# Kernel tuning notes

Measured on AMD Instinct MI355X. Metric: run time of the kernel, lower is better.

## Reference

```python
import jax, jax.numpy as jnp
import numpy as np

SCALING = 32.0 / 16.0  # alpha / rank

def setup_inputs() -> dict:
    key = jax.random.key(0)
    k1, k2, k3, k4, k5 = jax.random.split(key, 5)
    B, S, D_IN, D_OUT, R = 4, 2048, 4096, 4096, 16
    x = jax.random.normal(k1, (B, S, D_IN), dtype=jnp.float32)
    weight_int = jax.random.randint(k2, (D_OUT, D_IN), -128, 128, dtype=jnp.int32)
    weight_scale = jax.random.uniform(k3, (1,), dtype=jnp.float32) * 0.01 + 1e-4
    lora_A = jax.random.normal(k4, (R, D_IN), dtype=jnp.float32) * (1.0 / np.sqrt(D_IN))
    lora_B = jax.random.normal(k5, (D_OUT, R), dtype=jnp.float32) * 0.02
    return {"x": x, "weight_int": weight_int, "weight_scale": weight_scale,
            "lora_A": lora_A, "lora_B": lora_B}

def reference(x, weight_int, weight_scale, lora_A, lora_B):
    # Dequantized base weight: [out, in]
    w = weight_int.astype(jnp.float32) * weight_scale  # broadcast scalar scale
    base = jnp.einsum('bsi,oi->bso', x, w)
    # Low-rank LoRA path: (x @ A^T) @ B^T * scaling
    lora = jnp.einsum('bsr,or->bso', jnp.einsum('bsi,ri->bsr', x, lora_A), lora_B) * SCALING
    return base + lora
```

## Files before the change

### kernel.cpp

```cpp
#include <hip/hip_runtime.h>

constexpr int M = 8192;
constexpr int N = 4096;
constexpr int K = 4096;
constexpr float SCALING = 2.0f;

typedef __bf16 bf16x8 __attribute__((ext_vector_type(8)));
typedef __bf16 bf16x4 __attribute__((ext_vector_type(4)));
typedef float  f32x4  __attribute__((ext_vector_type(4)));

__global__ __launch_bounds__(256) void qlora_cast_x(const float* __restrict__ x,
                                                    __bf16* __restrict__ xb) {
    const size_t i = ((size_t)blockIdx.x * 256 + threadIdx.x) * 8;
    const float4 v0 = *(const float4*)(x + i);
    const float4 v1 = *(const float4*)(x + i + 4);
    bf16x8 o;
    o[0] = (__bf16)v0.x; o[1] = (__bf16)v0.y; o[2] = (__bf16)v0.z; o[3] = (__bf16)v0.w;
    o[4] = (__bf16)v1.x; o[5] = (__bf16)v1.y; o[6] = (__bf16)v1.z; o[7] = (__bf16)v1.w;
    *(bf16x8*)(xb + i) = o;
}

__global__ __launch_bounds__(256) void qlora_prep_w(const int* __restrict__ wi,
                                                    const float* __restrict__ wscale,
                                                    const float* __restrict__ lA,
                                                    const float* __restrict__ lB,
                                                    __bf16* __restrict__ W) {
    __shared__ __align__(16) float As[16][1028];
    const int t  = threadIdx.x;
    const int ol = t >> 4;
    const int kk = t & 15;
    const int o  = blockIdx.x * 16 + ol;
    const float s = wscale[0];
    float b[16];
#pragma unroll
    for (int r = 0; r < 16; ++r) b[r] = lB[o * 16 + r];

    for (int c = 0; c < 4; ++c) {
        const int c0 = c * 1024;
#pragma unroll
        for (int i = 0; i < 16; ++i) {
            const int idx = t + i * 256;
            const int r   = idx >> 8;
            const int c4  = idx & 255;
            const float4 v = *(const float4*)(lA + r * K + c0 + c4 * 4);
            *(float4*)(&As[r][c4 * 4]) = v;
        }
        __syncthreads();
#pragma unroll
        for (int j = 0; j < 16; ++j) {
            const int k4 = kk + j * 16;
            const int kg = c0 + k4 * 4;
            const int4 w4 = *(const int4*)(wi + (size_t)o * K + kg);
            float a0 = 0.f, a1 = 0.f, a2 = 0.f, a3 = 0.f;
#pragma unroll
            for (int r = 0; r < 16; ++r) {
                const float4 a4 = *(const float4*)(&As[r][k4 * 4]);
                a0 += b[r] * a4.x; a1 += b[r] * a4.y;
                a2 += b[r] * a4.z; a3 += b[r] * a4.w;
            }
            bf16x4 v;
            v[0] = (__bf16)((float)w4.x * s + SCALING * a0);
            v[1] = (__bf16)((float)w4.y * s + SCALING * a1);
            v[2] = (__bf16)((float)w4.z * s + SCALING * a2);
            v[3] = (__bf16)((float)w4.w * s + SCALING * a3);
            *(bf16x4*)(W + (size_t)o * K + kg) = v;
        }
        __syncthreads();
    }
}

__device__ __forceinline__ void async16(const __bf16* g, __bf16* l) {
    __builtin_amdgcn_global_load_lds(
        (const __attribute__((address_space(1))) unsigned int*)(unsigned long long)g,
        (__attribute__((address_space(3))) unsigned int*)(unsigned int)(unsigned long long)l,
        16, 0, 0);
}

__global__ __launch_bounds__(512, 2) void qlora_gemm_bt(const __bf16* __restrict__ A,
                                                        const __bf16* __restrict__ B,
                                                        float* __restrict__ C) {
    __shared__ __align__(16) __bf16 Lds[65536];

    const int tid  = threadIdx.x;
    const int w    = tid >> 6;
    const int lane = tid & 63;
    const int quad = lane >> 4;
    const int lb   = lane & 15;
    const int wm   = w >> 2;
    const int wn   = w & 3;

    const int swz = (blockIdx.x & 7) * 64 + (blockIdx.x >> 3);
    const int bx  = swz >> 5;
    const int by  = swz & 31;
    const size_t mBase = (size_t)by * 256;
    const size_t nBase = (size_t)bx * 256;

    const int r8 = lane >> 3;
    const int ch = ((lane & 7) ^ r8) * 8;
    const __bf16* gA = A + (mBase + w * 32 + r8) * K + ch;
    const __bf16* gB = B + (nBase + w * 32 + r8) * K + ch;
    __bf16* lA0 = Lds + w * 2048;
    __bf16* lB0 = Lds + 16384 + w * 2048;

    const int roA = (wm * 128 + lb) * 64;
    const int roB = (wn * 64 + lb) * 64;
    const int sw0 = ((0 + quad) ^ (lb & 7)) * 8;
    const int sw1 = ((4 + quad) ^ (lb & 7)) * 8;

    f32x4 acc[8][4] = {};

    auto stage = [&](int t) {
        const int b = t & 1;
        const size_t kt = (size_t)t * 64;
        const __bf16* pa = gA + kt;
        const __bf16* pb = gB + kt;
        __bf16* la = lA0 + b * 32768;
        __bf16* lbp = lB0 + b * 32768;
#pragma unroll
        for (int j = 0; j < 4; ++j) {
            async16(pa + (size_t)(j * 8) * K, la + j * 512);
            async16(pb + (size_t)(j * 8) * K, lbp + j * 512);
        }
    };

    auto MF = [](bf16x8 a, bf16x8 b, f32x4 c) {
        return __builtin_amdgcn_mfma_f32_16x16x32_bf16(a, b, c, 0, 0, 0);
    };

    stage(0);
    asm volatile("s_waitcnt vmcnt(0)" ::: "memory");
    __builtin_amdgcn_s_barrier();

#pragma unroll 2
    for (int t = 0; t < 64; ++t) {
        const __bf16* Ab = Lds + (t & 1) * 32768;
        const __bf16* Bb = Ab + 16384;

        bf16x8 af[4][2], b01[2][2], b23[2][2];

#pragma unroll
        for (int fm = 0; fm < 4; ++fm) {
            af[fm][0] = *(const bf16x8*)(Ab + roA + fm * 1024 + sw0);
            af[fm][1] = *(const bf16x8*)(Ab + roA + fm * 1024 + sw1);
        }
#pragma unroll
        for (int fn = 0; fn < 2; ++fn) {
            b01[fn][0] = *(const bf16x8*)(Bb + roB + fn * 1024 + sw0);
            b01[fn][1] = *(const bf16x8*)(Bb + roB + fn * 1024 + sw1);
        }
        if (t + 1 < 64) stage(t + 1);
        __builtin_amdgcn_s_barrier();
        asm volatile("s_waitcnt lgkmcnt(0)" ::: "memory");
        __builtin_amdgcn_s_setprio(1);
#pragma unroll
        for (int fm = 0; fm < 4; ++fm)
#pragma unroll
            for (int fn = 0; fn < 2; ++fn) {
                acc[fm][fn] = MF(af[fm][0], b01[fn][0], acc[fm][fn]);
                acc[fm][fn] = MF(af[fm][1], b01[fn][1], acc[fm][fn]);
            }
        __builtin_amdgcn_s_setprio(0);
        __builtin_amdgcn_s_barrier();

#pragma unroll
        for (int fn = 0; fn < 2; ++fn) {
            b23[fn][0] = *(const bf16x8*)(Bb + roB + (fn + 2) * 1024 + sw0);
            b23[fn][1] = *(const bf16x8*)(Bb + roB + (fn + 2) * 1024 + sw1);
        }
        __builtin_amdgcn_s_barrier();
        asm volatile("s_waitcnt lgkmcnt(0)" ::: "memory");
        __builtin_amdgcn_s_setprio(1);
#pragma unroll
        for (int fm = 0; fm < 4; ++fm)
#pragma unroll
            for (int fn = 0; fn < 2; ++fn) {
                acc[fm][fn + 2] = MF(af[fm][0], b23[fn][0], acc[fm][fn + 2]);
                acc[fm][fn + 2] = MF(af[fm][1], b23[fn][1], acc[fm][fn + 2]);
            }
        __builtin_amdgcn_s_setprio(0);
        __builtin_amdgcn_s_barrier();

#pragma unroll
        for (int fm = 0; fm < 4; ++fm) {
            af[fm][0] = *(const bf16x8*)(Ab + roA + (fm + 4) * 1024 + sw0);
            af[fm][1] = *(const bf16x8*)(Ab + roA + (fm + 4) * 1024 + sw1);
        }
        __builtin_amdgcn_s_barrier();
        asm volatile("s_waitcnt lgkmcnt(0)" ::: "memory");
        __builtin_amdgcn_s_setprio(1);
#pragma unroll
        for (int fm = 0; fm < 4; ++fm)
#pragma unroll
            for (int fn = 0; fn < 2; ++fn) {
                acc[fm + 4][fn] = MF(af[fm][0], b01[fn][0], acc[fm + 4][fn]);
                acc[fm + 4][fn] = MF(af[fm][1], b01[fn][1], acc[fm + 4][fn]);
            }
        __builtin_amdgcn_s_setprio(0);
        __builtin_amdgcn_s_barrier();

        __builtin_amdgcn_s_setprio(1);
#pragma unroll
        for (int fm = 0; fm < 4; ++fm)
#pragma unroll
            for (int fn = 0; fn < 2; ++fn) {
                acc[fm + 4][fn + 2] = MF(af[fm][0], b23[fn][0], acc[fm + 4][fn + 2]);
                acc[fm + 4][fn + 2] = MF(af[fm][1], b23[fn][1], acc[fm + 4][fn + 2]);
            }
        __builtin_amdgcn_s_setprio(0);
        asm volatile("s_waitcnt vmcnt(0)" ::: "memory");
        __builtin_amdgcn_s_barrier();
    }

#pragma unroll
    for (int fm = 0; fm < 8; ++fm) {
        const size_t m0 = mBase + wm * 128 + fm * 16 + quad * 4;
#pragma unroll
        for (int fn = 0; fn < 4; ++fn) {
            const size_t n0 = nBase + wn * 64 + fn * 16 + lb;
            float* p = C + m0 * N + n0;
            p[0 * (size_t)N] = acc[fm][fn][0];
            p[1 * (size_t)N] = acc[fm][fn][1];
            p[2 * (size_t)N] = acc[fm][fn][2];
            p[3 * (size_t)N] = acc[fm][fn][3];
        }
    }
}

extern "C" void kernel_launch(void* const* d_in, const int* in_sizes, int n_in,
                              void* d_out, int out_size, void* d_ws, size_t ws_size,
                              hipStream_t stream) {
    const float* x      = (const float*)d_in[0];
    const int*   wint   = (const int*)d_in[1];
    const float* wscale = (const float*)d_in[2];
    const float* lA     = (const float*)d_in[3];
    const float* lB     = (const float*)d_in[4];
    float* out = (float*)d_out;

    __bf16* Xb = (__bf16*)d_ws;
    __bf16* Wb = (__bf16*)((char*)d_ws + (size_t)M * K * 2);

    qlora_cast_x<<<16384, 256, 0, stream>>>(x, Xb);
    qlora_prep_w<<<256, 256, 0, stream>>>(wint, wscale, lA, lB, Wb);
    qlora_gemm_bt<<<dim3(512), dim3(512), 0, stream>>>(Xb, Wb, out);
}
```

Before: 521.7 us.

## Switch GEMM mainloop to 4-stage K=32 pipeline with deeper async prefetch

The GEMM mainloop moves from a double-buffered K=64 tile to a four-buffer ring of K=32 tiles. Three stages are prefetched ahead, and vmcnt waits are relaxed so global-to-LDS loads overlap more MFMA work. The LDS layout and swizzle change to 32-element rows and the loop is manually unrolled by four. The cost is twice as many iterations, each with the same number of barriers, and more complex wait accounting that could stall if the counts are off.

New measurement: 545.8 us. 4.6% more time.

```diff
diff --git a/kernel.cpp b/kernel.cpp
--- a/kernel.cpp
+++ b/kernel.cpp
@@ -95,121 +95,97 @@
     const size_t mBase = (size_t)by * 256;
     const size_t nBase = (size_t)bx * 256;
 
-    const int r8 = lane >> 3;
-    const int ch = ((lane & 7) ^ r8) * 8;
-    const __bf16* gA = A + (mBase + w * 32 + r8) * K + ch;
-    const __bf16* gB = B + (nBase + w * 32 + r8) * K + ch;
-    __bf16* lA0 = Lds + w * 2048;
-    __bf16* lB0 = Lds + 16384 + w * 2048;
-
-    const int roA = (wm * 128 + lb) * 64;
-    const int roB = (wn * 64 + lb) * 64;
-    const int sw0 = ((0 + quad) ^ (lb & 7)) * 8;
-    const int sw1 = ((4 + quad) ^ (lb & 7)) * 8;
+    const int r16 = lane >> 2;
+    const int ch  = ((lane & 3) ^ ((lane >> 3) & 3)) * 8;
+    const __bf16* gA = A + (mBase + w * 32 + r16) * K + ch;
+    const __bf16* gB = B + (nBase + w * 32 + r16) * K + ch;
+
+    const int sw  = (quad ^ ((lb >> 1) & 3)) * 8;
+    const int roA = (wm * 128 + lb) * 32 + sw;
+    const int roB = (wn * 64 + lb) * 32 + sw;
 
     f32x4 acc[8][4] = {};
 
-    auto stage = [&](int t) {
-        const int b = t & 1;
-        const size_t kt = (size_t)t * 64;
-        const __bf16* pa = gA + kt;
-        const __bf16* pb = gB + kt;
-        __bf16* la = lA0 + b * 32768;
-        __bf16* lbp = lB0 + b * 32768;
-#pragma unroll
-        for (int j = 0; j < 4; ++j) {
-            async16(pa + (size_t)(j * 8) * K, la + j * 512);
-            async16(pb + (size_t)(j * 8) * K, lbp + j * 512);
-        }
+    auto stage = [&](int buf, int s) {
+        __bf16* la  = Lds + buf * 16384 + w * 1024;
+        __bf16* lbp = la + 8192;
+        const __bf16* pa = gA + (size_t)s * 32;
+        const __bf16* pb = gB + (size_t)s * 32;
+        async16(pa, la);
+        async16(pa + (size_t)16 * K, la + 512);
+        async16(pb, lbp);
+        async16(pb + (size_t)16 * K, lbp + 512);
     };
 
     auto MF = [](bf16x8 a, bf16x8 b, f32x4 c) {
         return __builtin_amdgcn_mfma_f32_16x16x32_bf16(a, b, c, 0, 0, 0);
     };
 
-    stage(0);
-    asm volatile("s_waitcnt vmcnt(0)" ::: "memory");
+#define VM8 asm volatile("s_waitcnt vmcnt(8)" ::: "memory")
+#define VM4 asm volatile("s_waitcnt vmcnt(4)" ::: "memory")
+#define VM0 asm volatile("s_waitcnt vmcnt(0)" ::: "memory")
+#define NOWAIT ((void)0)
+
+#define GSTEP(BUF, DOSTAGE, SNEXT, WAITSTMT)                                 \
+  {                                                                          \
+    const __bf16* Ab = Lds + (BUF) * 16384;                                  \
+    const __bf16* Bb = Ab + 8192;                                            \
+    bf16x8 af[4], bfr[4];                                                    \
+    _Pragma("unroll")                                                        \
+    for (int fm = 0; fm < 4; ++fm)                                           \
+      af[fm] = *(const bf16x8*)(Ab + roA + fm * 512);                        \
+    _Pragma("unroll")                                                        \
+    for (int fn = 0; fn < 4; ++fn)                                           \
+      bfr[fn] = *(const bf16x8*)(Bb + roB + fn * 512);                       \
+    if (DOSTAGE) stage((SNEXT) & 3, (SNEXT));                                \
+    __builtin_amdgcn_s_barrier();                                            \
+    asm volatile("s_waitcnt lgkmcnt(0)" ::: "memory");                       \
+    __builtin_amdgcn_s_setprio(1);                                           \
+    _Pragma("unroll")                                                        \
+    for (int fm = 0; fm < 4; ++fm)                                           \
+      _Pragma("unroll")                                                      \
+      for (int fn = 0; fn < 4; ++fn)                                         \
+        acc[fm][fn] = MF(af[fm], bfr[fn], acc[fm][fn]);                      \
+    __builtin_amdgcn_s_setprio(0);                                           \
+    __builtin_amdgcn_s_barrier();                                            \
+    _Pragma("unroll")                                                        \
+    for (int fm = 0; fm < 4; ++fm)                                           \
+      af[fm] = *(const bf16x8*)(Ab + roA + (fm + 4) * 512);                  \
+    __builtin_amdgcn_s_barrier();                                            \
+    asm volatile("s_waitcnt lgkmcnt(0)" ::: "memory");                       \
+    __builtin_amdgcn_s_setprio(1);                                           \
+    _Pragma("unroll")                                                        \
+    for (int fm = 0; fm < 4; ++fm)                                           \
+      _Pragma("unroll")                                                      \
+      for (int fn = 0; fn < 4; ++fn)                                         \
+        acc[fm + 4][fn] = MF(af[fm], bfr[fn], acc[fm + 4][fn]);              \
+    __builtin_amdgcn_s_setprio(0);                                           \
+    WAITSTMT;                                                                \
+    __builtin_amdgcn_s_barrier();                                            \
+  }
+
+    stage(0, 0);
+    stage(1, 1);
+    stage(2, 2);
+    VM8;
     __builtin_amdgcn_s_barrier();
 
-#pragma unroll 2
-    for (int t = 0; t < 64; ++t) {
-        const __bf16* Ab = Lds + (t & 1) * 32768;
-        const __bf16* Bb = Ab + 16384;
-
-        bf16x8 af[4][2], b01[2][2], b23[2][2];
-
-#pragma unroll
-        for (int fm = 0; fm < 4; ++fm) {
-            af[fm][0] = *(const bf16x8*)(Ab + roA + fm * 1024 + sw0);
-            af[fm][1] = *(const bf16x8*)(Ab + roA + fm * 1024 + sw1);
-        }
-#pragma unroll
-        for (int fn = 0; fn < 2; ++fn) {
-            b01[fn][0] = *(const bf16x8*)(Bb + roB + fn * 1024 + sw0);
-            b01[fn][1] = *(const bf16x8*)(Bb + roB + fn * 1024 + sw1);
-        }
-        if (t + 1 < 64) stage(t + 1);
-        __builtin_amdgcn_s_barrier();
-        asm volatile("s_waitcnt lgkmcnt(0)" ::: "memory");
-        __builtin_amdgcn_s_setprio(1);
-#pragma unroll
-        for (int fm = 0; fm < 4; ++fm)
-#pragma unroll
-            for (int fn = 0; fn < 2; ++fn) {
-                acc[fm][fn] = MF(af[fm][0], b01[fn][0], acc[fm][fn]);
-                acc[fm][fn] = MF(af[fm][1], b01[fn][1], acc[fm][fn]);
-            }
-        __builtin_amdgcn_s_setprio(0);
-        __builtin_amdgcn_s_barrier();
-
-#pragma unroll
-        for (int fn = 0; fn < 2; ++fn) {
-            b23[fn][0] = *(const bf16x8*)(Bb + roB + (fn + 2) * 1024 + sw0);
-            b23[fn][1] = *(const bf16x8*)(Bb + roB + (fn + 2) * 1024 + sw1);
-        }
-        __builtin_amdgcn_s_barrier();
-        asm volatile("s_waitcnt lgkmcnt(0)" ::: "memory");
-        __builtin_amdgcn_s_setprio(1);
-#pragma unroll
-        for (int fm = 0; fm < 4; ++fm)
-#pragma unroll
-            for (int fn = 0; fn < 2; ++fn) {
-                acc[fm][fn + 2] = MF(af[fm][0], b23[fn][0], acc[fm][fn + 2]);
-                acc[fm][fn + 2] = MF(af[fm][1], b23[fn][1], acc[fm][fn + 2]);
-            }
-        __builtin_amdgcn_s_setprio(0);
-        __builtin_amdgcn_s_barrier();
-
-#pragma unroll
-        for (int fm = 0; fm < 4; ++fm) {
-            af[fm][0] = *(const bf16x8*)(Ab + roA + (fm + 4) * 1024 + sw0);
-            af[fm][1] = *(const bf16x8*)(Ab + roA + (fm + 4) * 1024 + sw1);
-        }
-        __builtin_amdgcn_s_barrier();
-        asm volatile("s_waitcnt lgkmcnt(0)" ::: "memory");
-        __builtin_amdgcn_s_setprio(1);
-#pragma unroll
-        for (int fm = 0; fm < 4; ++fm)
-#pragma unroll
-            for (int fn = 0; fn < 2; ++fn) {
-                acc[fm + 4][fn] = MF(af[fm][0], b01[fn][0], acc[fm + 4][fn]);
-                acc[fm + 4][fn] = MF(af[fm][1], b01[fn][1], acc[fm + 4][fn]);
-            }
-        __builtin_amdgcn_s_setprio(0);
-        __builtin_amdgcn_s_barrier();
-
-        __builtin_amdgcn_s_setprio(1);
-#pragma unroll
-        for (int fm = 0; fm < 4; ++fm)
-#pragma unroll
-            for (int fn = 0; fn < 2; ++fn) {
-                acc[fm + 4][fn + 2] = MF(af[fm][0], b23[fn][0], acc[fm + 4][fn + 2]);
-                acc[fm + 4][fn + 2] = MF(af[fm][1], b23[fn][1], acc[fm + 4][fn + 2]);
-            }
-        __builtin_amdgcn_s_setprio(0);
-        asm volatile("s_waitcnt vmcnt(0)" ::: "memory");
-        __builtin_amdgcn_s_barrier();
+    for (int s = 0; s < 124; s += 4) {
+        GSTEP(0, true, s + 3, VM8);
+        GSTEP(1, true, s + 4, VM8);
+        GSTEP(2, true, s + 5, VM8);
+        GSTEP(3, true, s + 6, VM8);
     }
+    GSTEP(0, true, 127, VM8);
+    GSTEP(1, false, 0, VM4);
+    GSTEP(2, false, 0, VM0);
+    GSTEP(3, false, 0, NOWAIT);
+
+#undef GSTEP
+#undef VM8
+#undef VM4
+#undef VM0
+#undef NOWAIT
 
 #pragma unroll
     for (int fm = 0; fm < 8; ++fm) {
```
